# Kernel optimization log

Measured on AMD Instinct MI355X. Metric: run time of the kernel, lower is better.

The kernel has to match this reference:

```python
import jax, jax.numpy as jnp
import numpy as np

MARGIN = 0.2
PAIR_EPS = 1e-6   # torch pairwise_distance eps inside TripletMarginLoss
NORM_EPS = 1e-12  # F.normalize eps


def setup_inputs() -> dict:
    key = jax.random.key(0)
    k1, k2, k3 = jax.random.split(key, 3)
    bs, C, D = 64, 1024, 64
    inputs = jax.random.normal(k1, (bs, C, D), dtype=jnp.float32)
    label = jax.random.randint(k2, (bs, C, 1), 0, 2).astype(jnp.float32)
    prot = jax.random.normal(k3, (C, D), dtype=jnp.float32)
    prot = prot / jnp.linalg.norm(prot, axis=1, keepdims=True)
    return {"inputs": inputs, "label": label, "pos_prot": prot, "only_update": 0}


def reference(inputs, label, pos_prot, only_update):
    bs, C, D = inputs.shape
    # F.normalize(p=2, dim=1) per class slice == normalize over last dim of [bs,C,D]
    nrm = jnp.linalg.norm(inputs, axis=-1, keepdims=True)
    x = inputs / jnp.maximum(nrm, NORM_EPS)                      # [bs,C,D]

    # torch.cdist(x, prot): euclidean distances [bs, C(anchor cls), C(prot)]
    x2 = jnp.sum(x * x, axis=-1)                                 # [bs,C]
    p2 = jnp.sum(pos_prot * pos_prot, axis=-1)                   # [C]
    xp = jnp.einsum('bcd,kd->bck', x, pos_prot)                  # [bs,C,C]
    d2 = x2[:, :, None] + p2[None, None, :] - 2.0 * xp
    prot_dist = jnp.sqrt(jnp.maximum(d2, 0.0))                   # [bs,C,C]

    # hard negative: nearest prototype excluding the anchor's own class
    # (argsort + skip-self loop == masked argmin)
    eye = jnp.eye(C, dtype=bool)[None, :, :]
    neg_cls = jnp.argmin(jnp.where(eye, jnp.inf, prot_dist), axis=-1)  # [bs,C]

    positives = pos_prot[None, :, :]                             # [1,C,D] (broadcast of repeat)
    negatives = pos_prot[neg_cls]                                # [bs,C,D]

    # TripletMarginLoss(margin=0.2, p=2, reduction='none'), eps inside distance
    d_ap = jnp.linalg.norm(x - positives + PAIR_EPS, axis=-1)    # [bs,C]
    d_an = jnp.linalg.norm(x - negatives + PAIR_EPS, axis=-1)    # [bs,C]
    tri = jnp.maximum(d_ap - d_an + MARGIN, 0.0)                 # [bs,C]

    w = label[:, :, 0]                                           # [bs,C]
    loss = jnp.mean(jnp.sum(tri * w, axis=-1) / jnp.sum(w, axis=-1))
    return loss
```

## Files before the change

### kernel.cpp

```cpp
#include <hip/hip_runtime.h>
#include <cfloat>

#define BS 64
#define C  1024
#define D  64
#define CT 128

typedef __attribute__((ext_vector_type(8))) short short8;
typedef __attribute__((ext_vector_type(4))) float f32x4;
typedef unsigned short ushort_t;
typedef unsigned int uint_t;

__device__ __forceinline__ ushort_t f2bf(float f) {
    uint_t u = __float_as_uint(f);
    u += 0x7fffu + ((u >> 16) & 1u);
    return (ushort_t)(u >> 16);
}

__global__ void prep_prot(const float* __restrict__ prot, ushort_t* __restrict__ ph)
{
    const int k = blockIdx.x * 128 + threadIdx.x;
    const float4* row = (const float4*)(prot + (size_t)k * D);
    const int jt = k >> 4;
    #pragma unroll
    for (int dg = 0; dg < 8; dg++) {
        float4 a = row[dg * 2];
        float4 b = row[dg * 2 + 1];
        float x[8] = {a.x, a.y, a.z, a.w, b.x, b.y, b.z, b.w};
        short8 hv;
        #pragma unroll
        for (int e = 0; e < 8; e++) hv[e] = (short)f2bf(x[e]);
        const int h  = dg >> 2;
        const int ln = (k & 15) + (dg & 3) * 16;
        ((short8*)ph)[(size_t)jt * 128 + h * 64 + ln] = hv;
    }
}

__global__ __launch_bounds__(512, 4)
void triplet_mfma(const float* __restrict__ inputs,
                  const float* __restrict__ label,
                  const float* __restrict__ prot,
                  const ushort_t* __restrict__ phg,
                  float* __restrict__ part)
{
    __shared__ short8 bsh[32 * 128];
    __shared__ uint_t redk[CT][4];
    __shared__ float  wred[16];

    const int tid  = threadIdx.x;
    const int lane = tid & 63;
    const int wid  = tid >> 6;
    const int wr   = wid >> 2;
    const int wc   = wid & 3;
    const int b    = blockIdx.x >> 3;
    const int c0   = (blockIdx.x & 7) * CT;

    const short8* BH = (const short8*)phg;

    #pragma unroll
    for (int it = 0; it < 2; it++) {
        const int rel = tid + it * 512;
        const int ft = rel >> 7, w = rel & 127, h = w >> 6, ln = w & 63;
        const int rr = ft * 16 + (ln & 15), dg = h * 4 + (ln >> 4);
        const float* s = inputs + (size_t)(b * C + c0 + rr) * D + dg * 8;
        float4 a  = *(const float4*)s;
        float4 b2 = *(const float4*)(s + 4);
        short8 hv;
        hv[0] = (short)f2bf(a.x);  hv[1] = (short)f2bf(a.y);
        hv[2] = (short)f2bf(a.z);  hv[3] = (short)f2bf(a.w);
        hv[4] = (short)f2bf(b2.x); hv[5] = (short)f2bf(b2.y);
        hv[6] = (short)f2bf(b2.z); hv[7] = (short)f2bf(b2.w);
        bsh[rel] = hv;
    }
    __syncthreads();

    short8 ah[4][2];
    #pragma unroll
    for (int i = 0; i < 4; i++) {
        ah[i][0] = bsh[(wr * 4 + i) * 128 + lane];
        ah[i][1] = bsh[(wr * 4 + i) * 128 + 64 + lane];
    }
    __syncthreads();

    uint_t bestk[16];
    #pragma unroll
    for (int q = 0; q < 16; q++) bestk[q] = 0u;

    const uint_t MMASK = 0xFFFFFC00u;
    const int rowtile0 = (c0 >> 4) + wr * 4;
    const int rsub = (lane >> 4) * 4;
    const int csub = lane & 15;

    auto process = [&](int jg, short8 b0, short8 b1) {
        const uint_t cidx = (uint_t)(1023 - (jg * 16 + csub));
        #pragma unroll
        for (int i = 0; i < 4; i++) {
            f32x4 acc = {16.f, 16.f, 16.f, 16.f};
            acc = __builtin_amdgcn_mfma_f32_16x16x32_bf16(ah[i][0], b0, acc, 0, 0, 0);
            acc = __builtin_amdgcn_mfma_f32_16x16x32_bf16(ah[i][1], b1, acc, 0, 0, 0);
            const bool dtile = (rowtile0 + i) == jg;
            #pragma unroll
            for (int r = 0; r < 4; r++) {
                uint_t key = (__float_as_uint(acc[r]) & MMASK) | cidx;
                if (dtile && (rsub + r) == csub) key = 0u;
                bestk[i * 4 + r] = bestk[i * 4 + r] > key ? bestk[i * 4 + r] : key;
            }
        }
    };

    for (int ch = 0; ch < 2; ch++) {
        if (ch) __syncthreads();
        const short8* src = BH + (size_t)ch * 4096;
        #pragma unroll
        for (int it = 0; it < 8; it++)
            bsh[it * 512 + tid] = src[it * 512 + tid];
        __syncthreads();

        const int base = wc * 8;
        short8 cb0 = bsh[(base + 0) * 128 + lane];
        short8 cb1 = bsh[(base + 0) * 128 + 64 + lane];
        #pragma unroll
        for (int lt = 0; lt < 8; lt++) {
            const int nt = (lt + 1 < 8) ? lt + 1 : 7;
            short8 n0 = bsh[(base + nt) * 128 + lane];
            short8 n1 = bsh[(base + nt) * 128 + 64 + lane];
            __builtin_amdgcn_sched_barrier(0);
            process(ch * 32 + base + lt, cb0, cb1);
            cb0 = n0; cb1 = n1;
        }
    }

    #pragma unroll
    for (int i = 0; i < 4; i++)
        #pragma unroll
        for (int r = 0; r < 4; r++) {
            uint_t v = bestk[i * 4 + r];
            #pragma unroll
            for (int off = 1; off < 16; off <<= 1) {
                uint_t ov = (uint_t)__shfl_xor((int)v, off);
                v = v > ov ? v : ov;
            }
            if (csub == 0) redk[wr * 64 + i * 16 + rsub + r][wc] = v;
        }
    __syncthreads();

    float num = 0.f, den = 0.f;
    {
        const int row = tid >> 2, p4 = tid & 3;
        uint_t kk = redk[row][p4];
        {
            uint_t o1 = (uint_t)__shfl_xor((int)kk, 1); kk = kk > o1 ? kk : o1;
            uint_t o2 = (uint_t)__shfl_xor((int)kk, 2); kk = kk > o2 ? kk : o2;
        }
        const int bi = 1023 - (int)(kk & 0x3FFu);
        const int cg = c0 + row;

        const float4* xr = (const float4*)(inputs + (size_t)(b * C + cg) * D) + p4 * 4;
        float4 xv[4];
        float x2 = 0.f;
        #pragma unroll
        for (int q = 0; q < 4; q++) {
            xv[q] = xr[q];
            x2 = fmaf(xv[q].x, xv[q].x, fmaf(xv[q].y, xv[q].y,
                 fmaf(xv[q].z, xv[q].z, fmaf(xv[q].w, xv[q].w, x2))));
        }
        x2 += __shfl_xor(x2, 1);
        x2 += __shfl_xor(x2, 2);
        const float inv = 1.0f / fmaxf(sqrtf(x2), 1e-12f);

        const float4* pp = (const float4*)(prot + (size_t)cg * D) + p4 * 4;
        const float4* pn = (const float4*)(prot + (size_t)bi * D) + p4 * 4;
        float sap = 0.f, san = 0.f;
        #pragma unroll
        for (int q = 0; q < 4; q++) {
            float4 aa = pp[q];
            float4 nn = pn[q];
            float t;
            t = fmaf(xv[q].x, inv, -aa.x) + 1e-6f;  sap = fmaf(t, t, sap);
            t = fmaf(xv[q].y, inv, -aa.y) + 1e-6f;  sap = fmaf(t, t, sap);
            t = fmaf(xv[q].z, inv, -aa.z) + 1e-6f;  sap = fmaf(t, t, sap);
            t = fmaf(xv[q].w, inv, -aa.w) + 1e-6f;  sap = fmaf(t, t, sap);
            t = fmaf(xv[q].x, inv, -nn.x) + 1e-6f;  san = fmaf(t, t, san);
            t = fmaf(xv[q].y, inv, -nn.y) + 1e-6f;  san = fmaf(t, t, san);
            t = fmaf(xv[q].z, inv, -nn.z) + 1e-6f;  san = fmaf(t, t, san);
            t = fmaf(xv[q].w, inv, -nn.w) + 1e-6f;  san = fmaf(t, t, san);
        }
        sap += __shfl_xor(sap, 1);  sap += __shfl_xor(sap, 2);
        san += __shfl_xor(san, 1);  san += __shfl_xor(san, 2);
        if (p4 == 0) {
            float tri = fmaxf(sqrtf(sap) - sqrtf(san) + 0.2f, 0.0f);
            float w   = label[b * C + cg];
            num = tri * w;
            den = w;
        }
    }

    #pragma unroll
    for (int off = 1; off < 64; off <<= 1) {
        num += __shfl_xor(num, off);
        den += __shfl_xor(den, off);
    }
    if (lane == 0) { wred[wid * 2] = num; wred[wid * 2 + 1] = den; }
    __syncthreads();

    if (tid == 0) {
        float sn = 0.f, sd = 0.f;
        #pragma unroll
        for (int wv = 0; wv < 8; wv++) { sn += wred[wv * 2]; sd += wred[wv * 2 + 1]; }
        part[blockIdx.x * 2 + 0] = sn;
        part[blockIdx.x * 2 + 1] = sd;
    }
}

__global__ void triplet_finish(const float* __restrict__ part, float* __restrict__ out)
{
    int t = threadIdx.x;
    float num = 0.f, den = 0.f;
    #pragma unroll
    for (int h = 0; h < 8; h++) {
        num += part[(t * 8 + h) * 2 + 0];
        den += part[(t * 8 + h) * 2 + 1];
    }
    float v = num / den;
    #pragma unroll
    for (int off = 32; off > 0; off >>= 1) v += __shfl_down(v, off);
    if (t == 0) out[0] = v * (1.0f / (float)BS);
}

extern "C" void kernel_launch(void* const* d_in, const int* in_sizes, int n_in,
                              void* d_out, int out_size, void* d_ws, size_t ws_size,
                              hipStream_t stream)
{
    const float* inputs = (const float*)d_in[0];
    const float* label  = (const float*)d_in[1];
    const float* prot   = (const float*)d_in[2];
    float* out = (float*)d_out;

    ushort_t* phg  = (ushort_t*)d_ws;
    float*    part = (float*)(phg + (size_t)C * D);

    prep_prot<<<dim3(C / 128), dim3(128), 0, stream>>>(prot, phg);
    triplet_mfma<<<dim3(BS * (C / CT)), dim3(512), 0, stream>>>(
        inputs, label, prot, phg, part);
    triplet_finish<<<1, 64, 0, stream>>>(part, out);
}
```

Baseline: 27.35 us.

## Split prototype range across two blocks and move loss into separate kernel

The fused kernel is split into two kernels. The key kernel launches twice as many blocks, each covering half of the prototype columns, and writes per-row packed argmax keys to workspace. A new loss kernel merges the two halves and computes the triplet loss and partial sums. The aim is more parallelism and shorter per-block work on the MFMA phase, at the cost of an extra kernel launch, re-reading the bf16 inputs conversion in each half block, and a global round trip for the keys.

Measured after the change: 57.38 us. +109.8%, slower.

```diff
diff --git a/kernel.cpp b/kernel.cpp
--- a/kernel.cpp
+++ b/kernel.cpp
@@ -37,23 +37,23 @@
 }
 
 __global__ __launch_bounds__(512, 4)
-void triplet_mfma(const float* __restrict__ inputs,
-                  const float* __restrict__ label,
-                  const float* __restrict__ prot,
+void triplet_keys(const float* __restrict__ inputs,
                   const ushort_t* __restrict__ phg,
-                  float* __restrict__ part)
+                  uint_t* __restrict__ pkeys)
 {
     __shared__ short8 bsh[32 * 128];
     __shared__ uint_t redk[CT][4];
-    __shared__ float  wred[16];
 
     const int tid  = threadIdx.x;
     const int lane = tid & 63;
     const int wid  = tid >> 6;
     const int wr   = wid >> 2;
     const int wc   = wid & 3;
-    const int b    = blockIdx.x >> 3;
-    const int c0   = (blockIdx.x & 7) * CT;
+    const int blk  = blockIdx.x;
+    const int kh   = blk & 1;
+    const int ct   = (blk >> 1) & 7;
+    const int b    = blk >> 4;
+    const int c0   = ct * CT;
 
     const short8* BH = (const short8*)phg;
 
@@ -82,6 +82,12 @@
     }
     __syncthreads();
 
+    const short8* src = BH + (size_t)kh * 4096;
+    #pragma unroll
+    for (int it = 0; it < 8; it++)
+        bsh[it * 512 + tid] = src[it * 512 + tid];
+    __syncthreads();
+
     uint_t bestk[16];
     #pragma unroll
     for (int q = 0; q < 16; q++) bestk[q] = 0u;
@@ -108,26 +114,17 @@
         }
     };
 
-    for (int ch = 0; ch < 2; ch++) {
-        if (ch) __syncthreads();
-        const short8* src = BH + (size_t)ch * 4096;
-        #pragma unroll
-        for (int it = 0; it < 8; it++)
-            bsh[it * 512 + tid] = src[it * 512 + tid];
-        __syncthreads();
-
-        const int base = wc * 8;
-        short8 cb0 = bsh[(base + 0) * 128 + lane];
-        short8 cb1 = bsh[(base + 0) * 128 + 64 + lane];
-        #pragma unroll
-        for (int lt = 0; lt < 8; lt++) {
-            const int nt = (lt + 1 < 8) ? lt + 1 : 7;
-            short8 n0 = bsh[(base + nt) * 128 + lane];
-            short8 n1 = bsh[(base + nt) * 128 + 64 + lane];
-            __builtin_amdgcn_sched_barrier(0);
-            process(ch * 32 + base + lt, cb0, cb1);
-            cb0 = n0; cb1 = n1;
-        }
+    const int base = wc * 8;
+    short8 cb0 = bsh[(base + 0) * 128 + lane];
+    short8 cb1 = bsh[(base + 0) * 128 + 64 + lane];
+    #pragma unroll
+    for (int lt = 0; lt < 8; lt++) {
+        const int nt = (lt + 1 < 8) ? lt + 1 : 7;
+        short8 n0 = bsh[(base + nt) * 128 + lane];
+        short8 n1 = bsh[(base + nt) * 128 + 64 + lane];
+        __builtin_amdgcn_sched_barrier(0);
+        process(kh * 32 + base + lt, cb0, cb1);
+        cb0 = n0; cb1 = n1;
     }
 
     #pragma unroll
@@ -144,18 +141,43 @@
         }
     __syncthreads();
 
+    if (tid < CT) {
+        uint_t k0 = redk[tid][0], k1 = redk[tid][1];
+        uint_t k2 = redk[tid][2], k3 = redk[tid][3];
+        uint_t kk = k0 > k1 ? k0 : k1;
+        uint_t kl = k2 > k3 ? k2 : k3;
+        kk = kk > kl ? kk : kl;
+        pkeys[(size_t)kh * (BS * C) + b * C + c0 + tid] = kk;
+    }
+}
+
+__global__ __launch_bounds__(512)
+void triplet_loss(const float* __restrict__ inputs,
+                  const float* __restrict__ label,
+                  const float* __restrict__ prot,
+                  const uint_t* __restrict__ pkeys,
+                  float* __restrict__ part)
+{
+    __shared__ float wred[16];
+
+    const int tid  = threadIdx.x;
+    const int lane = tid & 63;
+    const int wid  = tid >> 6;
+    const int blk  = blockIdx.x;
+    const int b    = blk >> 3;
+    const int c0   = (blk & 7) * CT;
+
     float num = 0.f, den = 0.f;
     {
         const int row = tid >> 2, p4 = tid & 3;
-        uint_t kk = redk[row][p4];
-        {
-            uint_t o1 = (uint_t)__shfl_xor((int)kk, 1); kk = kk > o1 ? kk : o1;
-            uint_t o2 = (uint_t)__shfl_xor((int)kk, 2); kk = kk > o2 ? kk : o2;
-        }
+        const int gr = b * C + c0 + row;
+        uint_t k0 = pkeys[gr];
+        uint_t k1 = pkeys[(size_t)(BS * C) + gr];
+        uint_t kk = k0 > k1 ? k0 : k1;
         const int bi = 1023 - (int)(kk & 0x3FFu);
         const int cg = c0 + row;
 
-        const float4* xr = (const float4*)(inputs + (size_t)(b * C + cg) * D) + p4 * 4;
+        const float4* xr = (const float4*)(inputs + (size_t)gr * D) + p4 * 4;
         float4 xv[4];
         float x2 = 0.f;
         #pragma unroll
@@ -207,8 +229,8 @@
         float sn = 0.f, sd = 0.f;
         #pragma unroll
         for (int wv = 0; wv < 8; wv++) { sn += wred[wv * 2]; sd += wred[wv * 2 + 1]; }
-        part[blockIdx.x * 2 + 0] = sn;
-        part[blockIdx.x * 2 + 1] = sd;
+        part[blk * 2 + 0] = sn;
+        part[blk * 2 + 1] = sd;
     }
 }
 
@@ -236,11 +258,13 @@
     const float* prot   = (const float*)d_in[2];
     float* out = (float*)d_out;
 
-    ushort_t* phg  = (ushort_t*)d_ws;
-    float*    part = (float*)(phg + (size_t)C * D);
+    ushort_t* phg   = (ushort_t*)d_ws;
+    uint_t*   pkeys = (uint_t*)(phg + (size_t)C * D);
+    float*    part  = (float*)(pkeys + 2 * BS * C);
 
     prep_prot<<<dim3(C / 128), dim3(128), 0, stream>>>(prot, phg);
-    triplet_mfma<<<dim3(BS * (C / CT)), dim3(512), 0, stream>>>(
-        inputs, label, prot, phg, part);
+    triplet_keys<<<dim3(BS * (C / CT) * 2), dim3(512), 0, stream>>>(inputs, phg, pkeys);
+    triplet_loss<<<dim3(BS * (C / CT)), dim3(512), 0, stream>>>(
+        inputs, label, prot, pkeys, part);
     triplet_finish<<<1, 64, 0, stream>>>(part, out);
 }
```

## Double-buffer prototype tiles in LDS using async global_load_lds

Applied to the files above, without the earlier changes.

Splits the single 64 KB LDS prototype buffer into two 32 KB halves and streams prototype tiles in four chunks. Each next chunk is fetched with global_load_lds direct-to-LDS loads while the MFMA argmin work runs on the current chunk. The first chunk's load is issued before the input bf16 conversion so the two overlap. The aim is to hide global-load latency and drop the register round-trip on the LDS fill. The cost is more chunks and barriers, plus reliance on the barrier correctly waiting for the async LDS writes.

New measurement: 27.06 us, median of 2. Within noise of the previous version (-1.1%).

```diff
diff --git a/kernel.cpp b/kernel.cpp
--- a/kernel.cpp
+++ b/kernel.cpp
@@ -43,7 +43,8 @@
                   const ushort_t* __restrict__ phg,
                   float* __restrict__ part)
 {
-    __shared__ short8 bsh[32 * 128];
+    __shared__ short8 bufA[2048];
+    __shared__ short8 bufB[2048];
     __shared__ uint_t redk[CT][4];
     __shared__ float  wred[16];
 
@@ -56,6 +57,18 @@
     const int c0   = (blockIdx.x & 7) * CT;
 
     const short8* BH = (const short8*)phg;
+
+    auto stage = [&](const short8* src, short8* dst) {
+        #pragma unroll
+        for (int it = 0; it < 4; it++) {
+            __builtin_amdgcn_global_load_lds(
+                (const __attribute__((address_space(1))) void*)(src + wid * 256 + it * 64 + lane),
+                (__attribute__((address_space(3))) void*)(dst + wid * 256 + it * 64),
+                16, 0, 0);
+        }
+    };
+
+    stage(BH, bufA);
 
     #pragma unroll
     for (int it = 0; it < 2; it++) {
@@ -70,15 +83,15 @@
         hv[2] = (short)f2bf(a.z);  hv[3] = (short)f2bf(a.w);
         hv[4] = (short)f2bf(b2.x); hv[5] = (short)f2bf(b2.y);
         hv[6] = (short)f2bf(b2.z); hv[7] = (short)f2bf(b2.w);
-        bsh[rel] = hv;
+        bufB[rel] = hv;
     }
     __syncthreads();
 
     short8 ah[4][2];
     #pragma unroll
     for (int i = 0; i < 4; i++) {
-        ah[i][0] = bsh[(wr * 4 + i) * 128 + lane];
-        ah[i][1] = bsh[(wr * 4 + i) * 128 + 64 + lane];
+        ah[i][0] = bufB[(wr * 4 + i) * 128 + lane];
+        ah[i][1] = bufB[(wr * 4 + i) * 128 + 64 + lane];
     }
     __syncthreads();
 
@@ -108,24 +121,21 @@
         }
     };
 
-    for (int ch = 0; ch < 2; ch++) {
-        if (ch) __syncthreads();
-        const short8* src = BH + (size_t)ch * 4096;
-        #pragma unroll
-        for (int it = 0; it < 8; it++)
-            bsh[it * 512 + tid] = src[it * 512 + tid];
+    for (int ch = 0; ch < 4; ch++) {
         __syncthreads();
-
-        const int base = wc * 8;
-        short8 cb0 = bsh[(base + 0) * 128 + lane];
-        short8 cb1 = bsh[(base + 0) * 128 + 64 + lane];
-        #pragma unroll
-        for (int lt = 0; lt < 8; lt++) {
-            const int nt = (lt + 1 < 8) ? lt + 1 : 7;
-            short8 n0 = bsh[(base + nt) * 128 + lane];
-            short8 n1 = bsh[(base + nt) * 128 + 64 + lane];
+        short8* cur = (ch & 1) ? bufB : bufA;
+        if (ch < 3) stage(BH + (size_t)(ch + 1) * 2048, (ch & 1) ? bufA : bufB);
+
+        const int base = wc * 4;
+        short8 cb0 = cur[(base + 0) * 128 + lane];
+        short8 cb1 = cur[(base + 0) * 128 + 64 + lane];
+        #pragma unroll
+        for (int lt = 0; lt < 4; lt++) {
+            const int nt = (lt + 1 < 4) ? lt + 1 : 3;
+            short8 n0 = cur[(base + nt) * 128 + lane];
+            short8 n1 = cur[(base + nt) * 128 + 64 + lane];
             __builtin_amdgcn_sched_barrier(0);
-            process(ch * 32 + base + lt, cb0, cb1);
+            process(ch * 16 + base + lt, cb0, cb1);
             cb0 = n0; cb1 = n1;
         }
     }
```
